# Performance work log

Hardware: AMD Instinct MI355X
Metric: run time of the kernel (lower is better)

The kernel has to match this reference:

```python
import jax, jax.numpy as jnp
import numpy as np

B, N, M, D, H, DH, DFF, L = 64, 2048, 32, 128, 4, 32, 512, 2
EPS = 1e-5


def setup_inputs() -> dict:
    key = jax.random.key(0)
    ks = jax.random.split(key, 8)
    def xav(k, shape, fan_in):
        return jax.random.normal(k, shape, jnp.float32) * (1.0 / np.sqrt(fan_in))
    return {
        "feat": jax.random.normal(ks[0], (B, N, D), jnp.float32),
        "I_pts": xav(ks[1], (L, M, D), D),                # inducing points per ISAB layer
        "Wq": xav(ks[2], (L, 2, D, H * DH), D),
        "Wk": xav(ks[3], (L, 2, D, H * DH), D),
        "Wv": xav(ks[4], (L, 2, D, H * DH), D),
        "Wo": xav(ks[5], (L, 2, H * DH, D), H * DH),
        "W1": xav(ks[6], (L, 2, D, DFF), D),
        "b1": jnp.zeros((L, 2, DFF), jnp.float32),
        "W2": xav(ks[7], (L, 2, DFF, D), DFF),
        "b2": jnp.zeros((L, 2, D), jnp.float32),
        "ln1_g": jnp.ones((L, 2, D), jnp.float32),
        "ln1_b": jnp.zeros((L, 2, D), jnp.float32),
        "ln2_g": jnp.ones((L, 2, D), jnp.float32),
        "ln2_b": jnp.zeros((L, 2, D), jnp.float32),
    }


def _layer_norm(x, g, b):
    mu = jnp.mean(x, axis=-1, keepdims=True)
    var = jnp.mean(jnp.square(x - mu), axis=-1, keepdims=True)
    return (x - mu) * jax.lax.rsqrt(var + EPS) * g + b


def _mha(q_feat, kv_feat, Wq, Wk, Wv, Wo, W1, b1, W2, b2, g1, be1, g2, be2):
    # q_feat: [B, nq, D], kv_feat: [B, nk, D]
    nq, nk = q_feat.shape[1], kv_feat.shape[1]
    Q = (q_feat @ Wq).reshape(B, nq, H, DH)
    K = (kv_feat @ Wk).reshape(B, nk, H, DH)
    V = (kv_feat @ Wv).reshape(B, nk, H, DH)
    # edge score = sum_d(q*k)/sqrt(d_head); edge_softmax normalizes over kv per query
    scores = jnp.einsum('bqhd,bkhd->bhqk', Q, K) / np.sqrt(DH)
    att = jax.nn.softmax(scores, axis=-1)
    out = jnp.einsum('bhqk,bkhd->bqhd', att, V).reshape(B, nq, H * DH)
    sa = out @ Wo
    x = _layer_norm(q_feat + sa, g1, be1)
    ffn = jax.nn.relu(x @ W1 + b1) @ W2 + b2
    return _layer_norm(x + ffn, g2, be2)


def reference(feat, I_pts, Wq, Wk, Wv, Wo, W1, b1, W2, b2, ln1_g, ln1_b, ln2_g, ln2_b):
    x = feat
    for l in range(L):  # ISAB layers
        query = jnp.broadcast_to(I_pts[l], (B, M, D))
        kv = x
        for j in range(2):  # induced -> set, then set -> induced
            rst = _mha(query, kv,
                       Wq[l, j], Wk[l, j], Wv[l, j], Wo[l, j],
                       W1[l, j], b1[l, j], W2[l, j], b2[l, j],
                       ln1_g[l, j], ln1_b[l, j], ln2_g[l, j], ln2_b[l, j])
            query, kv = kv, rst
        x = rst
    return x
```

## Files before the change

### kernel.cpp

```cpp
#include <hip/hip_runtime.h>
#include <hip/hip_bf16.h>

#define BB 64
#define NN 2048
#define MM 32
#define DD 128
#define HH 4
#define LL 2
#define BN (BB*NN)
#define BM (BB*MM)

typedef short bf16x8 __attribute__((ext_vector_type(8)));
typedef float f32x4 __attribute__((ext_vector_type(4)));
typedef unsigned int u32;
#define MFMA __builtin_amdgcn_mfma_f32_16x16x32_bf16

__device__ __forceinline__ unsigned short f2bf(float f){
  __hip_bfloat16 h = __float2bfloat16(f);
  unsigned short u;
  __builtin_memcpy(&u, &h, 2);
  return u;
}
__device__ __forceinline__ float bf2f(unsigned short u){
  union { u32 u; float f; } v; v.u = ((u32)u) << 16; return v.f;
}
__device__ __forceinline__ u32 pack2(float a, float b){
  return (u32)f2bf(a) | ((u32)f2bf(b) << 16);
}
__device__ __forceinline__ float ldf(const float* p){ return *p; }
__device__ __forceinline__ float ldf(const unsigned short* p){ return bf2f(*p); }
__device__ __forceinline__ void stf(float* p, float v){ *p = v; }
__device__ __forceinline__ void stf(unsigned short* p, float v){ *p = f2bf(v); }

__device__ __forceinline__ f32x4 ld4(const float* p){ return *reinterpret_cast<const f32x4*>(p); }
__device__ __forceinline__ f32x4 ld4(const unsigned short* p){
  ushort4 u = *reinterpret_cast<const ushort4*>(p);
  f32x4 r; r[0]=bf2f(u.x); r[1]=bf2f(u.y); r[2]=bf2f(u.z); r[3]=bf2f(u.w); return r;
}
__device__ __forceinline__ void st4(float* p, f32x4 v){ *reinterpret_cast<f32x4*>(p) = v; }
__device__ __forceinline__ void st4(unsigned short* p, f32x4 v){
  ushort4 u; u.x=f2bf(v[0]); u.y=f2bf(v[1]); u.z=f2bf(v[2]); u.w=f2bf(v[3]);
  *reinterpret_cast<ushort4*>(p) = u;
}

__device__ __forceinline__ bf16x8 cvt8(const float* __restrict__ p){
  float4 a = *reinterpret_cast<const float4*>(p);
  float4 b = *reinterpret_cast<const float4*>(p + 4);
  bf16x8 r;
  r[0]=(short)f2bf(a.x); r[1]=(short)f2bf(a.y); r[2]=(short)f2bf(a.z); r[3]=(short)f2bf(a.w);
  r[4]=(short)f2bf(b.x); r[5]=(short)f2bf(b.y); r[6]=(short)f2bf(b.z); r[7]=(short)f2bf(b.w);
  return r;
}

template<int NW>
__device__ __forceinline__ void stage_img(const unsigned short* __restrict__ img,
                                          unsigned short* Wt){
  int wave = threadIdx.x >> 6, lane = threadIdx.x & 63;
  #pragma unroll
  for (int i = 0; i < 32/NW; i++){
    int off = ((i*NW + wave) << 9);
    const unsigned short* gp = img + off + lane*8;
    unsigned short* lp = Wt + off;
    __builtin_amdgcn_global_load_lds(
        (__attribute__((address_space(1))) void*)gp,
        (__attribute__((address_space(3))) void*)lp, 16, 0, 0);
  }
}

__device__ __forceinline__ bf16x8 bfrag(const unsigned short* Wt, int cb, int k0, int lane){
  int c = (cb << 4) + (lane & 15);
  int kk = (k0 + ((lane >> 4) << 3)) ^ ((c & 7) << 3);
  return *reinterpret_cast<const bf16x8*>(Wt + (c << 7) + kk);
}

__device__ __forceinline__ void load_afrag(const float* __restrict__ A, int r0, int lane,
                                           bf16x8 af[2][4]){
  int li = lane & 15, lg = lane >> 4;
  #pragma unroll
  for (int s = 0; s < 2; s++){
    const float* ap = A + (size_t)(r0 + s*16 + li) * 128 + (lg << 3);
    #pragma unroll
    for (int ks = 0; ks < 4; ks++) af[s][ks] = cvt8(ap + ks*32);
  }
}
__device__ __forceinline__ void load_afrag(const unsigned short* __restrict__ A, int r0,
                                           int lane, bf16x8 af[2][4]){
  int li = lane & 15, lg = lane >> 4;
  #pragma unroll
  for (int s = 0; s < 2; s++){
    const unsigned short* ap = A + (size_t)(r0 + s*16 + li) * 128 + (lg << 3);
    #pragma unroll
    for (int ks = 0; ks < 4; ks++) af[s][ks] = *reinterpret_cast<const bf16x8*>(ap + ks*32);
  }
}

__device__ __forceinline__ void mfma_tile32(const bf16x8 af[2][4], const unsigned short* Wt,
                                            int lane, f32x4 acc[2][8]){
  #pragma unroll
  for (int ks = 0; ks < 4; ks++){
    #pragma unroll
    for (int cb = 0; cb < 8; cb++){
      bf16x8 b = bfrag(Wt, cb, ks*32, lane);
      acc[0][cb] = MFMA(af[0][ks], b, acc[0][cb], 0, 0, 0);
      acc[1][cb] = MFMA(af[1][ks], b, acc[1][cb], 0, 0, 0);
    }
  }
}
__device__ __forceinline__ void mfma_swp(const bf16x8 af[2][4], const unsigned short* Wt,
                                         int lane, f32x4 acc[2][8]){
  #pragma unroll
  for (int ks = 0; ks < 4; ks++){
    #pragma unroll
    for (int cb = 0; cb < 8; cb++){
      bf16x8 w = bfrag(Wt, cb, ks*32, lane);
      acc[0][cb] = MFMA(w, af[0][ks], acc[0][cb], 0, 0, 0);
      acc[1][cb] = MFMA(w, af[1][ks], acc[1][cb], 0, 0, 0);
    }
  }
}

__device__ __forceinline__ void zero_acc(f32x4 acc[2][8]){
  #pragma unroll
  for (int s = 0; s < 2; s++)
    #pragma unroll
    for (int cb = 0; cb < 8; cb++) acc[s][cb] = (f32x4){0.f,0.f,0.f,0.f};
}

__device__ __forceinline__ void store_f32(const f32x4 acc[2][8], float* __restrict__ C,
                                          int r0, int lane){
  int li = lane & 15, lg = lane >> 4;
  #pragma unroll
  for (int s = 0; s < 2; s++)
    #pragma unroll
    for (int q = 0; q < 4; q++){
      float* crow = C + (size_t)(r0 + s*16 + lg*4 + q) * 128;
      #pragma unroll
      for (int cb = 0; cb < 8; cb++) crow[cb*16 + li] = acc[s][cb][q];
    }
}
__device__ __forceinline__ void store_bf16(const f32x4 acc[2][8], unsigned short* __restrict__ C,
                                           int r0, int lane){
  int li = lane & 15, lg = lane >> 4;
  #pragma unroll
  for (int s = 0; s < 2; s++)
    #pragma unroll
    for (int q = 0; q < 4; q++){
      unsigned short* crow = C + (size_t)(r0 + s*16 + lg*4 + q) * 128;
      #pragma unroll
      for (int cb = 0; cb < 8; cb++) crow[cb*16 + li] = f2bf(acc[s][cb][q]);
    }
}
__device__ __forceinline__ void store_st2(const f32x4 acc[2][8], unsigned short* __restrict__ St2,
                                          int b, int jb, int lane){
  int li = lane & 15, lg = lane >> 4;
  #pragma unroll
  for (int s = 0; s < 2; s++)
    #pragma unroll
    for (int cb = 0; cb < 8; cb++){
      unsigned short* p = St2 + ((size_t)(b*128 + cb*16 + li))*2048 + jb + s*16 + lg*4;
      st4(p, acc[s][cb]);
    }
}

template<typename RT, typename OT>
__device__ __forceinline__ void ln_ep(const f32x4 acc[8], const float* __restrict__ bias,
    const RT* __restrict__ resid, unsigned int resmask,
    const float* __restrict__ g, const float* __restrict__ beta,
    OT* __restrict__ C, int r0, int lane){
  int li = lane & 15, lg = lane >> 4;
  float gv[8], bv[8], biasv[8];
  #pragma unroll
  for (int cb = 0; cb < 8; cb++){
    int col = cb*16 + li;
    gv[cb] = g[col]; bv[cb] = beta[col];
    biasv[cb] = bias ? bias[col] : 0.f;
  }
  #pragma unroll
  for (int q = 0; q < 4; q++){
    int r = r0 + lg*4 + q;
    const RT* rrow = resid + (size_t)(r & resmask) * 128;
    float v[8], sum = 0.f, ss = 0.f;
    #pragma unroll
    for (int cb = 0; cb < 8; cb++){
      float x = acc[cb][q] + biasv[cb] + ldf(rrow + cb*16 + li);
      v[cb] = x; sum += x; ss += x*x;
    }
    #pragma unroll
    for (int mk = 1; mk < 16; mk <<= 1){ sum += __shfl_xor(sum, mk); ss += __shfl_xor(ss, mk); }
    float mu = sum * (1.f/128.f);
    float var = ss * (1.f/128.f) - mu*mu;
    float rs = rsqrtf(var + 1e-5f);
    OT* crow = C + (size_t)r * 128;
    #pragma unroll
    for (int cb = 0; cb < 8; cb++)
      stf(crow + cb*16 + li, (v[cb] - mu) * rs * gv[cb] + bv[cb]);
  }
}

template<typename RT, typename OT>
__device__ __forceinline__ void ln_swp(const f32x4 accO[2][8], const float* __restrict__ bias,
    const RT* __restrict__ resid, const float* __restrict__ g, const float* __restrict__ beta,
    OT* __restrict__ C, int r0, int lane){
  int li = lane & 15, lg = lane >> 4;
  #pragma unroll
  for (int s = 0; s < 2; s++){
    int r = r0 + s*16 + li;
    const RT* rr = resid + (size_t)r * 128;
    float v[8][4]; float sum = 0.f, ss = 0.f;
    #pragma unroll
    for (int cb = 0; cb < 8; cb++){
      int c0 = cb*16 + lg*4;
      f32x4 rq = ld4(rr + c0);
      f32x4 bq = bias ? *reinterpret_cast<const f32x4*>(bias + c0) : (f32x4){0.f,0.f,0.f,0.f};
      #pragma unroll
      for (int q = 0; q < 4; q++){
        float x = accO[s][cb][q] + bq[q] + rq[q];
        v[cb][q] = x; sum += x; ss += x*x;
      }
    }
    sum += __shfl_xor(sum, 16); ss += __shfl_xor(ss, 16);
    sum += __shfl_xor(sum, 32); ss += __shfl_xor(ss, 32);
    float mu = sum * (1.f/128.f);
    float var = ss * (1.f/128.f) - mu*mu;
    float rs = rsqrtf(var + 1e-5f);
    OT* co = C + (size_t)r * 128;
    #pragma unroll
    for (int cb = 0; cb < 8; cb++){
      int c0 = cb*16 + lg*4;
      f32x4 gq = *reinterpret_cast<const f32x4*>(g + c0);
      f32x4 tq = *reinterpret_cast<const f32x4*>(beta + c0);
      f32x4 o;
      #pragma unroll
      for (int q = 0; q < 4; q++) o[q] = (v[cb][q] - mu) * rs * gq[q] + tq[q];
      st4(co + c0, o);
    }
  }
}

__device__ __forceinline__ bf16x8 redist(const u32 pk[2][8][2], int s, int ks,
                                         int t, int srcA, int srcB){
  u32 a0 = (u32)__shfl((int)pk[s][2*ks][0],   srcA);
  u32 a1 = (u32)__shfl((int)pk[s][2*ks+1][0], srcA);
  u32 a2 = (u32)__shfl((int)pk[s][2*ks][1],   srcA);
  u32 a3 = (u32)__shfl((int)pk[s][2*ks+1][1], srcA);
  u32 b0 = (u32)__shfl((int)pk[s][2*ks][0],   srcB);
  u32 b1 = (u32)__shfl((int)pk[s][2*ks+1][0], srcB);
  u32 b2 = (u32)__shfl((int)pk[s][2*ks][1],   srcB);
  u32 b3 = (u32)__shfl((int)pk[s][2*ks+1][1], srcB);
  union { u32 u[4]; bf16x8 v; } r;
  r.u[0] = t ? a1 : a0;
  r.u[1] = t ? a3 : a2;
  r.u[2] = t ? b1 : b0;
  r.u[3] = t ? b3 : b2;
  return r.v;
}


__global__ __launch_bounds__(256) void cvt_bf16(const float* __restrict__ in,
                                                unsigned short* __restrict__ out){
  size_t i = ((size_t)blockIdx.x*256 + threadIdx.x) * 8;
  float4 a = *reinterpret_cast<const float4*>(in + i);
  float4 b = *reinterpret_cast<const float4*>(in + i + 4);
  ushort4 u0; u0.x=f2bf(a.x); u0.y=f2bf(a.y); u0.z=f2bf(a.z); u0.w=f2bf(a.w);
  ushort4 u1; u1.x=f2bf(b.x); u1.y=f2bf(b.y); u1.z=f2bf(b.z); u1.w=f2bf(b.w);
  *reinterpret_cast<ushort4*>(out + i) = u0;
  *reinterpret_cast<ushort4*>(out + i + 4) = u1;
}

__global__ __launch_bounds__(256) void prep_imgs(const float* __restrict__ Wq,
    const float* __restrict__ Wk, const float* __restrict__ Wv, const float* __restrict__ Wo,
    const float* __restrict__ W1, const float* __restrict__ W2, unsigned short* __restrict__ imgs){
  int slot = blockIdx.x;
  const float* src; int ldw;
  if (slot < 16){
    int j = slot >> 2, m = slot & 3;
    const float* base = (m==0) ? Wq : (m==1) ? Wk : (m==2) ? Wv : Wo;
    src = base + j*16384; ldw = 128;
  } else if (slot < 32){
    int s = slot - 16; int j = s >> 2, dc = s & 3;
    src = W1 + j*65536 + dc*128; ldw = 512;
  } else {
    int s = slot - 32; int j = s >> 2, dc = s & 3;
    src = W2 + j*65536 + dc*16384; ldw = 128;
  }
  unsigned short* img = imgs + (size_t)slot * 16384;
  for (int i = threadIdx.x; i < 16384; i += 256){
    int k = i >> 7, c = i & 127;
    img[(c << 7) + (k ^ ((c & 7) << 3))] = f2bf(src[k*ldw + c]);
  }
}

__global__ __launch_bounds__(256) void prep_phaseA(const float* __restrict__ I,
    const float* __restrict__ Wq, const float* __restrict__ Wk, unsigned short* __restrict__ WfImg){
  __shared__ float Qi[32*128];
  for (int i = threadIdx.x; i < 4096; i += 256){
    int q = i >> 7, c = i & 127;
    float s = 0.f;
    #pragma unroll 8
    for (int d = 0; d < 128; d++) s += I[q*128 + d] * Wq[d*128 + c];
    Qi[i] = s;
  }
  __syncthreads();
  const float scale = 0.17677669529663687f;
  for (int i = threadIdx.x; i < 1024; i += 256){
    int k = (blockIdx.x << 3) + (i >> 7), c = i & 127;
    int hc = c >> 5, qc = c & 31;
    float s = 0.f;
    #pragma unroll
    for (int d = 0; d < 32; d++) s += Wk[k*128 + hc*32 + d] * Qi[qc*128 + hc*32 + d];
    WfImg[(c << 7) + (k ^ ((c & 7) << 3))] = f2bf(s * scale);
  }
}

__global__ __launch_bounds__(256) void prep_phaseB(const float* __restrict__ Wq,
    const float* __restrict__ Wo, const float* __restrict__ Khb, const float* __restrict__ Vhb,
    unsigned short* __restrict__ WfImgs, unsigned short* __restrict__ GvImgs){
  __shared__ float Ks[32*129];
  __shared__ float Vs[32*129];
  __shared__ float Wqt[128*33];
  __shared__ float Wot[128*17];
  int b = blockIdx.x >> 3, part = blockIdx.x & 7;
  int hwf = part >> 1;
  for (int i = threadIdx.x; i < 4096; i += 256){
    int k = i >> 7, c = i & 127;
    Ks[k*129 + c] = Khb[b*4096 + i];
    Vs[k*129 + c] = Vhb[b*4096 + i];
  }
  for (int i = threadIdx.x; i < 4096; i += 256){
    int ci = i >> 5, d = i & 31;
    Wqt[ci*33 + d] = Wq[ci*128 + hwf*32 + d];
  }
  for (int i = threadIdx.x; i < 2048; i += 256){
    int row = i >> 4, cl = i & 15;
    Wot[row*17 + cl] = Wo[row*128 + part*16 + cl];
  }
  __syncthreads();
  const float scale = 0.17677669529663687f;
  unsigned short* wf = WfImgs + (size_t)b*16384;
  unsigned short* gv = GvImgs + (size_t)b*16384;
  {
    int ci = threadIdx.x & 127;
    float wq[32];
    #pragma unroll
    for (int d = 0; d < 32; d++) wq[d] = Wqt[ci*33 + d];
    #pragma unroll
    for (int it = 0; it < 8; it++){
      int kp = part*16 + (threadIdx.x >> 7) + it*2;
      int k = kp & 31;
      float s = 0.f;
      #pragma unroll
      for (int d = 0; d < 32; d++) s += wq[d] * Ks[k*129 + hwf*32 + d];
      wf[(kp << 7) + (ci ^ ((kp & 7) << 3))] = f2bf(s * scale);
    }
  }
  {
    int kp = threadIdx.x & 127;
    int h = kp >> 5, k = kp & 31;
    float vv[32];
    #pragma unroll
    for (int d = 0; d < 32; d++) vv[d] = Vs[k*129 + h*32 + d];
    #pragma unroll
    for (int it = 0; it < 8; it++){
      int c = part*16 + (threadIdx.x >> 7) + it*2;
      int cl = c & 15;
      float s = 0.f;
      #pragma unroll
      for (int d = 0; d < 32; d++) s += vv[d] * Wot[(h*32 + d)*17 + cl];
      gv[(c << 7) + (kp ^ ((c & 7) << 3))] = f2bf(s);
    }
  }
}

template<typename TX>
__global__ __launch_bounds__(512) void gemm_dual(const TX* __restrict__ X,
    const unsigned short* __restrict__ img0, const unsigned short* __restrict__ img1,
    unsigned short* __restrict__ St2, unsigned short* __restrict__ Vb){
  __shared__ __align__(16) unsigned short W0[16384];
  __shared__ __align__(16) unsigned short W1s[16384];
  stage_img<8>(img0, W0);
  stage_img<8>(img1, W1s);
  __syncthreads();
  int lane = threadIdx.x & 63, wave = threadIdx.x >> 6;
  int r0 = blockIdx.x*256 + wave*32;
  int b = r0 >> 11, jb = r0 & 2047;
  bf16x8 af[2][4];
  load_afrag(X, r0, lane, af);
  f32x4 acc[2][8];
  zero_acc(acc);
  mfma_tile32(af, W0, lane, acc);
  store_st2(acc, St2, b, jb, lane);
  zero_acc(acc);
  mfma_tile32(af, W1s, lane, acc);
  store_bf16(acc, Vb, r0, lane);
}

__global__ __launch_bounds__(256) void gemm_img(const float* __restrict__ A,
    const unsigned short* __restrict__ img, float* __restrict__ C){
  __shared__ __align__(16) unsigned short Wt[16384];
  stage_img<4>(img, Wt);
  __syncthreads();
  int lane = threadIdx.x & 63, wave = threadIdx.x >> 6;
  int r0 = blockIdx.x*128 + wave*32;
  bf16x8 af[2][4];
  load_afrag(A, r0, lane, af);
  f32x4 acc[2][8];
  zero_acc(acc);
  mfma_tile32(af, Wt, lane, acc);
  store_f32(acc, C, r0, lane);
}

__global__ __launch_bounds__(256) void gemm_ln_f32A(const float* __restrict__ A,
    const unsigned short* __restrict__ img, const float* __restrict__ resid, unsigned int resmask,
    const float* __restrict__ g, const float* __restrict__ beta, float* __restrict__ C){
  __shared__ __align__(16) unsigned short Wt[16384];
  stage_img<4>(img, Wt);
  __syncthreads();
  int lane = threadIdx.x & 63, wave = threadIdx.x >> 6;
  int r0 = blockIdx.x*128 + wave*32;
  bf16x8 af[2][4];
  load_afrag(A, r0, lane, af);
  f32x4 acc[2][8];
  zero_acc(acc);
  mfma_tile32(af, Wt, lane, acc);
  ln_ep(acc[0], nullptr, resid, resmask, g, beta, C, r0,      lane);
  ln_ep(acc[1], nullptr, resid, resmask, g, beta, C, r0 + 16, lane);
}

__global__ __launch_bounds__(512) void attn_pv(const unsigned short* __restrict__ St2,
    const unsigned short* __restrict__ V, float* __restrict__ O){
  __shared__ __align__(16) unsigned short Vt[2][4096];
  __shared__ __align__(16) float Ocomb[4][64][4];
  __shared__ float scomb[4][16];
  int b = blockIdx.x >> 2, h = blockIdx.x & 3;
  int lane = threadIdx.x & 63, w = threadIdx.x >> 6;
  int li = lane & 15, lg = lane >> 4;
  int qh = w & 1, dh = (w >> 1) & 1, jh = w >> 2;
  int tq = w & 3;
  const unsigned short* Sp = St2 + ((size_t)(b*128 + h*32 + qh*16 + li)) * 2048 + jh*1024;
  const unsigned short* Vb = V + (size_t)b*NN*128 + h*32;
  unsigned short* VtJ = Vt[jh];
  int vrow = tq*32 + (lane >> 2);
  int vd0  = (lane & 3) * 8;
  const unsigned short* vsrc = Vb + ((size_t)(jh*1024 + vrow))*128 + vd0;

  f32x4 acc = (f32x4){0.f,0.f,0.f,0.f};
  float s = 0.f;
  bf16x8 Ar[2][4];
  bf16x8 vr[2][2];

  #pragma unroll
  for (int t = 0; t < 2; t++)
    vr[0][t] = *reinterpret_cast<const bf16x8*>(vsrc + (size_t)t*16*128);
  #pragma unroll
  for (int ks = 0; ks < 4; ks++)
    Ar[0][ks] = *reinterpret_cast<const bf16x8*>(Sp + ks*32 + lg*8);

  #pragma unroll
  for (int c = 0; c < 8; c++){
    const int cur = c & 1, nxt = cur ^ 1;
    __syncthreads();
    #pragma unroll
    for (int t = 0; t < 2; t++){
      int jl = vrow + t*16;
      #pragma unroll
      for (int e = 0; e < 8; e++){
        int d = vd0 + e;
        VtJ[(d << 7) + (jl ^ ((d & 7) << 3))] = (unsigned short)vr[cur][t][e];
      }
    }
    __syncthreads();
    if (c < 7){
      #pragma unroll
      for (int t = 0; t < 2; t++)
        vr[nxt][t] = *reinterpret_cast<const bf16x8*>(vsrc + ((size_t)(c+1)*128 + t*16)*128);
      #pragma unroll
      for (int ks = 0; ks < 4; ks++)
        Ar[nxt][ks] = *reinterpret_cast<const bf16x8*>(Sp + (c+1)*128 + ks*32 + lg*8);
    }
    #pragma unroll
    for (int ks = 0; ks < 4; ks++){
      bf16x8 a;
      #pragma unroll
      for (int e = 0; e < 8; e++){
        float pv = __expf(fminf(bf2f((unsigned short)Ar[cur][ks][e]), 60.f));
        s += pv; a[e] = (short)f2bf(pv);
      }
      bf16x8 bb = bfrag(VtJ, dh, ks*32, lane);
      acc = MFMA(a, bb, acc, 0, 0, 0);
    }
  }
  s += __shfl_xor(s, 16);
  s += __shfl_xor(s, 32);
  if (jh == 1){
    *reinterpret_cast<f32x4*>(&Ocomb[tq][lane][0]) = acc;
    if (lg == 0) scomb[tq][li] = s;
  }
  __syncthreads();
  if (jh == 0){
    acc += *reinterpret_cast<const f32x4*>(&Ocomb[tq][lane][0]);
    float inv = 1.f / (s + scomb[tq][li]);
    float* op = O + ((size_t)(b*MM + qh*16))*128 + h*32 + dh*16 + li;
    #pragma unroll
    for (int r = 0; r < 4; r++){
      float iv = __shfl(inv, lg*4 + r);
      op[(size_t)(lg*4 + r)*128] = acc[r] * iv;
    }
  }
}

template<typename TX>
__global__ __launch_bounds__(512, 2) void attn_swp(const TX* __restrict__ X,
    const unsigned short* __restrict__ WfImgs, const unsigned short* __restrict__ GvImgs,
    const float* __restrict__ g, const float* __restrict__ beta,
    unsigned short* __restrict__ X1){
  __shared__ __align__(16) unsigned short WtF[16384];
  __shared__ __align__(16) unsigned short WtG[16384];
  int b = blockIdx.x >> 3;
  stage_img<8>(WfImgs + (size_t)b*16384, WtF);
  stage_img<8>(GvImgs + (size_t)b*16384, WtG);
  int lane = threadIdx.x & 63, wave = threadIdx.x >> 6;
  int li = lane & 15, lg = lane >> 4;
  int r0 = blockIdx.x*256 + wave*32;
  bf16x8 af[2][4];
  load_afrag(X, r0, lane, af);
  __syncthreads();
  f32x4 sv[2][8];
  zero_acc(sv);
  mfma_swp(af, WtF, lane, sv);
  u32 pk[2][8][2];
  #pragma unroll
  for (int s = 0; s < 2; s++)
    #pragma unroll
    for (int h = 0; h < 4; h++){
      float p[8];
      #pragma unroll
      for (int q = 0; q < 4; q++){ p[q] = sv[s][2*h][q]; p[4+q] = sv[s][2*h+1][q]; }
      float m = fmaxf(fmaxf(fmaxf(p[0],p[1]),fmaxf(p[2],p[3])),
                      fmaxf(fmaxf(p[4],p[5]),fmaxf(p[6],p[7])));
      m = fmaxf(m, __shfl_xor(m, 16));
      m = fmaxf(m, __shfl_xor(m, 32));
      float sm = 0.f;
      #pragma unroll
      for (int i = 0; i < 8; i++){ p[i] = __expf(p[i] - m); sm += p[i]; }
      sm += __shfl_xor(sm, 16);
      sm += __shfl_xor(sm, 32);
      float inv = 1.f / sm;
      pk[s][2*h][0]   = pack2(p[0]*inv, p[1]*inv);
      pk[s][2*h][1]   = pack2(p[2]*inv, p[3]*inv);
      pk[s][2*h+1][0] = pack2(p[4]*inv, p[5]*inv);
      pk[s][2*h+1][1] = pack2(p[6]*inv, p[7]*inv);
    }
  int t = lg >> 1;
  int srcA = li + (((lane >> 4) & 1) << 5);
  int srcB = srcA + 16;
  f32x4 accO[2][8];
  zero_acc(accO);
  #pragma unroll
  for (int ks = 0; ks < 4; ks++){
    bf16x8 hb0 = redist(pk, 0, ks, t, srcA, srcB);
    bf16x8 hb1 = redist(pk, 1, ks, t, srcA, srcB);
    #pragma unroll
    for (int cb = 0; cb < 8; cb++){
      bf16x8 w = bfrag(WtG, cb, ks*32, lane);
      accO[0][cb] = MFMA(w, hb0, accO[0][cb], 0, 0, 0);
      accO[1][cb] = MFMA(w, hb1, accO[1][cb], 0, 0, 0);
    }
  }
  ln_swp(accO, nullptr, X, g, beta, X1, r0, lane);
}

template<typename TA, typename TO>
__global__ __launch_bounds__(512, 2) void ffn_swp(const TA* __restrict__ X,
    const unsigned short* __restrict__ W1i, const float* __restrict__ b1,
    const unsigned short* __restrict__ W2i, const float* __restrict__ b2,
    const float* __restrict__ g, const float* __restrict__ beta,
    TO* __restrict__ OUT){
  __shared__ __align__(16) unsigned short Wt0[16384];
  __shared__ __align__(16) unsigned short Wt1[16384];
  int lane = threadIdx.x & 63, wave = threadIdx.x >> 6;
  int li = lane & 15, lg = lane >> 4;
  int r0 = blockIdx.x*256 + wave*32;
  bf16x8 af[2][4];
  load_afrag(X, r0, lane, af);
  f32x4 accO[2][8];
  zero_acc(accO);
  stage_img<8>(W1i, Wt0);
  stage_img<8>(W2i, Wt1);
  __syncthreads();
  int t = lg >> 1;
  int srcA = li + (((lane >> 4) & 1) << 5);
  int srcB = srcA + 16;
  for (int dc = 0; dc < 4; dc++){
    f32x4 acc1[2][8];
    zero_acc(acc1);
    mfma_swp(af, Wt0, lane, acc1);
    u32 pk[2][8][2];
    #pragma unroll
    for (int s = 0; s < 2; s++)
      #pragma unroll
      for (int cb = 0; cb < 8; cb++){
        f32x4 bq = *reinterpret_cast<const f32x4*>(b1 + dc*128 + cb*16 + lg*4);
        float v0 = fmaxf(acc1[s][cb][0] + bq[0], 0.f);
        float v1 = fmaxf(acc1[s][cb][1] + bq[1], 0.f);
        float v2 = fmaxf(acc1[s][cb][2] + bq[2], 0.f);
        float v3 = fmaxf(acc1[s][cb][3] + bq[3], 0.f);
        pk[s][cb][0] = pack2(v0, v1);
        pk[s][cb][1] = pack2(v2, v3);
      }
    __syncthreads();
    if (dc < 3) stage_img<8>(W1i + (dc+1)*16384, Wt0);
    #pragma unroll
    for (int ks = 0; ks < 4; ks++){
      bf16x8 hb0 = redist(pk, 0, ks, t, srcA, srcB);
      bf16x8 hb1 = redist(pk, 1, ks, t, srcA, srcB);
      #pragma unroll
      for (int cb = 0; cb < 8; cb++){
        bf16x8 w = bfrag(Wt1, cb, ks*32, lane);
        accO[0][cb] = MFMA(w, hb0, accO[0][cb], 0, 0, 0);
        accO[1][cb] = MFMA(w, hb1, accO[1][cb], 0, 0, 0);
      }
    }
    __syncthreads();
    if (dc < 3) stage_img<8>(W2i + (dc+1)*16384, Wt1);
  }
  ln_swp(accO, b2, X, g, beta, OUT, r0, lane);
}

extern "C" void kernel_launch(void* const* d_in, const int* in_sizes, int n_in,
                              void* d_out, int out_size, void* d_ws, size_t ws_size,
                              hipStream_t stream){
  (void)in_sizes; (void)n_in; (void)out_size;
  const float* feat = (const float*)d_in[0];
  const float* Ipts = (const float*)d_in[1];
  const float* Wq   = (const float*)d_in[2];
  const float* Wk   = (const float*)d_in[3];
  const float* Wv   = (const float*)d_in[4];
  const float* Wo   = (const float*)d_in[5];
  const float* W1   = (const float*)d_in[6];
  const float* b1   = (const float*)d_in[7];
  const float* W2   = (const float*)d_in[8];
  const float* b2   = (const float*)d_in[9];
  const float* g1   = (const float*)d_in[10];
  const float* be1  = (const float*)d_in[11];
  const float* g2   = (const float*)d_in[12];
  const float* be2  = (const float*)d_in[13];
  float* out = (float*)d_out;

  unsigned short* St2  = (unsigned short*)d_ws;
  unsigned short* bigX1 = St2;
  unsigned short* bigV = St2 + (size_t)BN*128;
  float* Oind  = (float*)(bigV + (size_t)BN*128);
  float* x1ind = Oind  + (size_t)BM*128;
  float* Hind  = x1ind + (size_t)BM*128;
  float* Khb   = Hind  + (size_t)BM*128;
  float* Vhb   = Khb   + (size_t)BM*128;
  unsigned short* imgs = (unsigned short*)(Vhb + (size_t)BM*128);

  unsigned short* imgQKVO = imgs;
  unsigned short* imgW1   = imgs + (size_t)16*16384;
  unsigned short* imgW2   = imgs + (size_t)32*16384;
  unsigned short* imgWf   = imgs + (size_t)48*16384;
  unsigned short* wfB     = imgs + (size_t)50*16384;
  unsigned short* gvB     = imgs + (size_t)114*16384;
  unsigned short* xb      = imgs + (size_t)178*16384;
  size_t need = (size_t)((char*)(xb + (size_t)BN*128) - (char*)d_ws);
  bool useXb = (ws_size >= need);

  prep_imgs<<<48, 256, 0, stream>>>(Wq, Wk, Wv, Wo, W1, W2, imgs);
  if (useXb)
    cvt_bf16<<<BN*128/8/256, 256, 0, stream>>>(feat, xb);

  for (int l = 0; l < LL; l++){
    const float* xf = (l == 0) ? feat : out;
    bool xBf = useXb;
    const float* Il = Ipts + l*MM*DD;
    int j0 = l*2, j1 = l*2 + 1;
    prep_phaseA<<<16, 256, 0, stream>>>(Il, Wq + j0*16384, Wk + j0*16384, imgWf + l*16384);
    if (xBf)
      gemm_dual<unsigned short><<<BN/256, 512, 0, stream>>>(xb, imgWf + l*16384,
          imgQKVO + (j0*4+2)*16384, St2, bigV);
    else
      gemm_dual<float><<<BN/256, 512, 0, stream>>>(xf, imgWf + l*16384,
          imgQKVO + (j0*4+2)*16384, St2, bigV);
    attn_pv<<<BB*HH, 512, 0, stream>>>(St2, bigV, Oind);
    gemm_ln_f32A<<<BM/128, 256, 0, stream>>>(Oind, imgQKVO + (j0*4+3)*16384, Il, 31u,
                                             g1 + j0*128, be1 + j0*128, x1ind);
    ffn_swp<float, float><<<BM/256, 512, 0, stream>>>(x1ind, imgW1 + (size_t)j0*4*16384,
        b1 + j0*512, imgW2 + (size_t)j0*4*16384, b2 + j0*128,
        g2 + j0*128, be2 + j0*128, Hind);
    gemm_img<<<BM/128, 256, 0, stream>>>(Hind, imgQKVO + (j1*4+1)*16384, Khb);
    gemm_img<<<BM/128, 256, 0, stream>>>(Hind, imgQKVO + (j1*4+2)*16384, Vhb);
    prep_phaseB<<<BB*8, 256, 0, stream>>>(Wq + j1*16384, Wo + j1*16384, Khb, Vhb, wfB, gvB);
    if (xBf)
      attn_swp<unsigned short><<<BN/256, 512, 0, stream>>>(xb, wfB, gvB,
          g1 + j1*128, be1 + j1*128, bigX1);
    else
      attn_swp<float><<<BN/256, 512, 0, stream>>>(xf, wfB, gvB,
          g1 + j1*128, be1 + j1*128, bigX1);
    if (l == 0 && useXb)
      ffn_swp<unsigned short, unsigned short><<<BN/256, 512, 0, stream>>>(bigX1,
          imgW1 + (size_t)j1*4*16384, b1 + j1*512, imgW2 + (size_t)j1*4*16384, b2 + j1*128,
          g2 + j1*128, be2 + j1*128, xb);
    else
      ffn_swp<unsigned short, float><<<BN/256, 512, 0, stream>>>(bigX1,
          imgW1 + (size_t)j1*4*16384, b1 + j1*512, imgW2 + (size_t)j1*4*16384, b2 + j1*128,
          g2 + j1*128, be2 + j1*128, out);
  }
}
```

Before: 552.8 us.

## Fuse set-side attention and FFN into one kernel, keeping x1 in registers

Merges the attn_swp and ffn_swp kernels for the N-sized set into a single attn_ffn kernel. The post-attention LayerNorm output is packed to bf16 in registers and fed straight into the FFN as both the GEMM A-operand and the residual. This removes the global write and re-read of the intermediate bigX1 buffer, and one kernel launch. In exchange, it holds extra packed state (pkX1) live across the FFN loop, which raises register pressure under the 512-thread, 2-block launch bounds and could cause spills.

```diff
diff --git a/kernel.cpp b/kernel.cpp
--- a/kernel.cpp
+++ b/kernel.cpp
@@ -508,67 +508,6 @@
   }
 }
 
-template<typename TX>
-__global__ __launch_bounds__(512, 2) void attn_swp(const TX* __restrict__ X,
-    const unsigned short* __restrict__ WfImgs, const unsigned short* __restrict__ GvImgs,
-    const float* __restrict__ g, const float* __restrict__ beta,
-    unsigned short* __restrict__ X1){
-  __shared__ __align__(16) unsigned short WtF[16384];
-  __shared__ __align__(16) unsigned short WtG[16384];
-  int b = blockIdx.x >> 3;
-  stage_img<8>(WfImgs + (size_t)b*16384, WtF);
-  stage_img<8>(GvImgs + (size_t)b*16384, WtG);
-  int lane = threadIdx.x & 63, wave = threadIdx.x >> 6;
-  int li = lane & 15, lg = lane >> 4;
-  int r0 = blockIdx.x*256 + wave*32;
-  bf16x8 af[2][4];
-  load_afrag(X, r0, lane, af);
-  __syncthreads();
-  f32x4 sv[2][8];
-  zero_acc(sv);
-  mfma_swp(af, WtF, lane, sv);
-  u32 pk[2][8][2];
-  #pragma unroll
-  for (int s = 0; s < 2; s++)
-    #pragma unroll
-    for (int h = 0; h < 4; h++){
-      float p[8];
-      #pragma unroll
-      for (int q = 0; q < 4; q++){ p[q] = sv[s][2*h][q]; p[4+q] = sv[s][2*h+1][q]; }
-      float m = fmaxf(fmaxf(fmaxf(p[0],p[1]),fmaxf(p[2],p[3])),
-                      fmaxf(fmaxf(p[4],p[5]),fmaxf(p[6],p[7])));
-      m = fmaxf(m, __shfl_xor(m, 16));
-      m = fmaxf(m, __shfl_xor(m, 32));
-      float sm = 0.f;
-      #pragma unroll
-      for (int i = 0; i < 8; i++){ p[i] = __expf(p[i] - m); sm += p[i]; }
-      sm += __shfl_xor(sm, 16);
-      sm += __shfl_xor(sm, 32);
-      float inv = 1.f / sm;
-      pk[s][2*h][0]   = pack2(p[0]*inv, p[1]*inv);
-      pk[s][2*h][1]   = pack2(p[2]*inv, p[3]*inv);
-      pk[s][2*h+1][0] = pack2(p[4]*inv, p[5]*inv);
-      pk[s][2*h+1][1] = pack2(p[6]*inv, p[7]*inv);
-    }
-  int t = lg >> 1;
-  int srcA = li + (((lane >> 4) & 1) << 5);
-  int srcB = srcA + 16;
-  f32x4 accO[2][8];
-  zero_acc(accO);
-  #pragma unroll
-  for (int ks = 0; ks < 4; ks++){
-    bf16x8 hb0 = redist(pk, 0, ks, t, srcA, srcB);
-    bf16x8 hb1 = redist(pk, 1, ks, t, srcA, srcB);
-    #pragma unroll
-    for (int cb = 0; cb < 8; cb++){
-      bf16x8 w = bfrag(WtG, cb, ks*32, lane);
-      accO[0][cb] = MFMA(w, hb0, accO[0][cb], 0, 0, 0);
-      accO[1][cb] = MFMA(w, hb1, accO[1][cb], 0, 0, 0);
-    }
-  }
-  ln_swp(accO, nullptr, X, g, beta, X1, r0, lane);
-}
-
 template<typename TA, typename TO>
 __global__ __launch_bounds__(512, 2) void ffn_swp(const TA* __restrict__ X,
     const unsigned short* __restrict__ W1i, const float* __restrict__ b1,
@@ -624,6 +563,178 @@
     if (dc < 3) stage_img<8>(W2i + (dc+1)*16384, Wt1);
   }
   ln_swp(accO, b2, X, g, beta, OUT, r0, lane);
+}
+
+template<typename TX, typename TO>
+__global__ __launch_bounds__(512, 2) void attn_ffn(const TX* __restrict__ X,
+    const unsigned short* __restrict__ WfImgs, const unsigned short* __restrict__ GvImgs,
+    const float* __restrict__ g1v, const float* __restrict__ be1v,
+    const unsigned short* __restrict__ W1i, const float* __restrict__ b1,
+    const unsigned short* __restrict__ W2i, const float* __restrict__ b2,
+    const float* __restrict__ g2v, const float* __restrict__ be2v,
+    TO* __restrict__ OUT){
+  __shared__ __align__(16) unsigned short Wt0[16384];
+  __shared__ __align__(16) unsigned short Wt1[16384];
+  int b = blockIdx.x >> 3;
+  stage_img<8>(WfImgs + (size_t)b*16384, Wt0);
+  stage_img<8>(GvImgs + (size_t)b*16384, Wt1);
+  int lane = threadIdx.x & 63, wave = threadIdx.x >> 6;
+  int li = lane & 15, lg = lane >> 4;
+  int r0 = blockIdx.x*256 + wave*32;
+  int t = lg >> 1;
+  int srcA = li + (((lane >> 4) & 1) << 5);
+  int srcB = srcA + 16;
+  bf16x8 af[2][4];
+  load_afrag(X, r0, lane, af);
+  __syncthreads();
+  f32x4 accO[2][8];
+  zero_acc(accO);
+  mfma_swp(af, Wt0, lane, accO);
+  u32 pkP[2][8][2];
+  #pragma unroll
+  for (int s = 0; s < 2; s++)
+    #pragma unroll
+    for (int h = 0; h < 4; h++){
+      float p[8];
+      #pragma unroll
+      for (int q = 0; q < 4; q++){ p[q] = accO[s][2*h][q]; p[4+q] = accO[s][2*h+1][q]; }
+      float m = fmaxf(fmaxf(fmaxf(p[0],p[1]),fmaxf(p[2],p[3])),
+                      fmaxf(fmaxf(p[4],p[5]),fmaxf(p[6],p[7])));
+      m = fmaxf(m, __shfl_xor(m, 16));
+      m = fmaxf(m, __shfl_xor(m, 32));
+      float sm = 0.f;
+      #pragma unroll
+      for (int i = 0; i < 8; i++){ p[i] = __expf(p[i] - m); sm += p[i]; }
+      sm += __shfl_xor(sm, 16);
+      sm += __shfl_xor(sm, 32);
+      float inv = 1.f / sm;
+      pkP[s][2*h][0]   = pack2(p[0]*inv, p[1]*inv);
+      pkP[s][2*h][1]   = pack2(p[2]*inv, p[3]*inv);
+      pkP[s][2*h+1][0] = pack2(p[4]*inv, p[5]*inv);
+      pkP[s][2*h+1][1] = pack2(p[6]*inv, p[7]*inv);
+    }
+  zero_acc(accO);
+  #pragma unroll
+  for (int ks = 0; ks < 4; ks++){
+    bf16x8 hb0 = redist(pkP, 0, ks, t, srcA, srcB);
+    bf16x8 hb1 = redist(pkP, 1, ks, t, srcA, srcB);
+    #pragma unroll
+    for (int cb = 0; cb < 8; cb++){
+      bf16x8 w = bfrag(Wt1, cb, ks*32, lane);
+      accO[0][cb] = MFMA(w, hb0, accO[0][cb], 0, 0, 0);
+      accO[1][cb] = MFMA(w, hb1, accO[1][cb], 0, 0, 0);
+    }
+  }
+  __syncthreads();
+  stage_img<8>(W1i, Wt0);
+  stage_img<8>(W2i, Wt1);
+  u32 pkX1[2][8][2];
+  #pragma unroll
+  for (int s = 0; s < 2; s++){
+    int r = r0 + s*16 + li;
+    const TX* rr = X + (size_t)r * 128;
+    float v[8][4]; float sum = 0.f, ss = 0.f;
+    #pragma unroll
+    for (int cb = 0; cb < 8; cb++){
+      int c0 = cb*16 + lg*4;
+      f32x4 rq = ld4(rr + c0);
+      #pragma unroll
+      for (int q = 0; q < 4; q++){
+        float x = accO[s][cb][q] + rq[q];
+        v[cb][q] = x; sum += x; ss += x*x;
+      }
+    }
+    sum += __shfl_xor(sum, 16); ss += __shfl_xor(ss, 16);
+    sum += __shfl_xor(sum, 32); ss += __shfl_xor(ss, 32);
+    float mu = sum * (1.f/128.f);
+    float var = ss * (1.f/128.f) - mu*mu;
+    float rs = rsqrtf(var + 1e-5f);
+    #pragma unroll
+    for (int cb = 0; cb < 8; cb++){
+      int c0 = cb*16 + lg*4;
+      f32x4 gq = *reinterpret_cast<const f32x4*>(g1v + c0);
+      f32x4 tq = *reinterpret_cast<const f32x4*>(be1v + c0);
+      float x0 = (v[cb][0] - mu)*rs*gq[0] + tq[0];
+      float x1 = (v[cb][1] - mu)*rs*gq[1] + tq[1];
+      float x2 = (v[cb][2] - mu)*rs*gq[2] + tq[2];
+      float x3 = (v[cb][3] - mu)*rs*gq[3] + tq[3];
+      pkX1[s][cb][0] = pack2(x0, x1);
+      pkX1[s][cb][1] = pack2(x2, x3);
+    }
+  }
+  bf16x8 af2[2][4];
+  #pragma unroll
+  for (int s = 0; s < 2; s++)
+    #pragma unroll
+    for (int ks = 0; ks < 4; ks++)
+      af2[s][ks] = redist(pkX1, s, ks, t, srcA, srcB);
+  __syncthreads();
+  zero_acc(accO);
+  for (int dc = 0; dc < 4; dc++){
+    f32x4 acc1[2][8];
+    zero_acc(acc1);
+    mfma_swp(af2, Wt0, lane, acc1);
+    u32 pk[2][8][2];
+    #pragma unroll
+    for (int s = 0; s < 2; s++)
+      #pragma unroll
+      for (int cb = 0; cb < 8; cb++){
+        f32x4 bq = *reinterpret_cast<const f32x4*>(b1 + dc*128 + cb*16 + lg*4);
+        float v0 = fmaxf(acc1[s][cb][0] + bq[0], 0.f);
+        float v1 = fmaxf(acc1[s][cb][1] + bq[1], 0.f);
+        float v2 = fmaxf(acc1[s][cb][2] + bq[2], 0.f);
+        float v3 = fmaxf(acc1[s][cb][3] + bq[3], 0.f);
+        pk[s][cb][0] = pack2(v0, v1);
+        pk[s][cb][1] = pack2(v2, v3);
+      }
+    __syncthreads();
+    if (dc < 3) stage_img<8>(W1i + (dc+1)*16384, Wt0);
+    #pragma unroll
+    for (int ks = 0; ks < 4; ks++){
+      bf16x8 hb0 = redist(pk, 0, ks, t, srcA, srcB);
+      bf16x8 hb1 = redist(pk, 1, ks, t, srcA, srcB);
+      #pragma unroll
+      for (int cb = 0; cb < 8; cb++){
+        bf16x8 w = bfrag(Wt1, cb, ks*32, lane);
+        accO[0][cb] = MFMA(w, hb0, accO[0][cb], 0, 0, 0);
+        accO[1][cb] = MFMA(w, hb1, accO[1][cb], 0, 0, 0);
+      }
+    }
+    __syncthreads();
+    if (dc < 3) stage_img<8>(W2i + (dc+1)*16384, Wt1);
+  }
+  #pragma unroll
+  for (int s = 0; s < 2; s++){
+    int r = r0 + s*16 + li;
+    float v[8][4]; float sum = 0.f, ss = 0.f;
+    #pragma unroll
+    for (int cb = 0; cb < 8; cb++){
+      int c0 = cb*16 + lg*4;
+      f32x4 bq = *reinterpret_cast<const f32x4*>(b2 + c0);
+      #pragma unroll
+      for (int q = 0; q < 4; q++){
+        float resid = bf2f((unsigned short)((pkX1[s][cb][q>>1] >> ((q&1)*16)) & 0xFFFFu));
+        float x = accO[s][cb][q] + bq[q] + resid;
+        v[cb][q] = x; sum += x; ss += x*x;
+      }
+    }
+    sum += __shfl_xor(sum, 16); ss += __shfl_xor(ss, 16);
+    sum += __shfl_xor(sum, 32); ss += __shfl_xor(ss, 32);
+    float mu = sum * (1.f/128.f);
+    float var = ss * (1.f/128.f) - mu*mu;
+    float rs = rsqrtf(var + 1e-5f);
+    TO* co = OUT + (size_t)r * 128;
+    #pragma unroll
+    for (int cb = 0; cb < 8; cb++){
+      int c0 = cb*16 + lg*4;
+      f32x4 gq = *reinterpret_cast<const f32x4*>(g2v + c0);
+      f32x4 tq = *reinterpret_cast<const f32x4*>(be2v + c0);
+      f32x4 o;
+      #pragma unroll
+      for (int q = 0; q < 4; q++) o[q] = (v[cb][q] - mu) * rs * gq[q] + tq[q];
+      st4(co + c0, o);
+    }
+  }
 }
 
 extern "C" void kernel_launch(void* const* d_in, const int* in_sizes, int n_in,
@@ -647,7 +758,6 @@
   float* out = (float*)d_out;
 
   unsigned short* St2  = (unsigned short*)d_ws;
-  unsigned short* bigX1 = St2;
   unsigned short* bigV = St2 + (size_t)BN*128;
   float* Oind  = (float*)(bigV + (size_t)BN*128);
   float* x1ind = Oind  + (size_t)BM*128;
@@ -691,19 +801,17 @@
     gemm_img<<<BM/128, 256, 0, stream>>>(Hind, imgQKVO + (j1*4+1)*16384, Khb);
     gemm_img<<<BM/128, 256, 0, stream>>>(Hind, imgQKVO + (j1*4+2)*16384, Vhb);
     prep_phaseB<<<BB*8, 256, 0, stream>>>(Wq + j1*16384, Wo + j1*16384, Khb, Vhb, wfB, gvB);
-    if (xBf)
-      attn_swp<unsigned short><<<BN/256, 512, 0, stream>>>(xb, wfB, gvB,
-          g1 + j1*128, be1 + j1*128, bigX1);
+    if (l == 0 && useXb)
+      attn_ffn<unsigned short, unsigned short><<<BN/256, 512, 0, stream>>>(xb, wfB, gvB,
+          g1 + j1*128, be1 + j1*128, imgW1 + (size_t)j1*4*16384, b1 + j1*512,
+          imgW2 + (size_t)j1*4*16384, b2 + j1*128, g2 + j1*128, be2 + j1*128, xb);
+    else if (useXb)
+      attn_ffn<unsigned short, float><<<BN/256, 512, 0, stream>>>(xb, wfB, gvB,
+          g1 + j1*128, be1 + j1*128, imgW1 + (size_t)j1*4*16384, b1 + j1*512,
+          imgW2 + (size_t)j1*4*16384, b2 + j1*128, g2 + j1*128, be2 + j1*128, out);
     else
-      attn_swp<float><<<BN/256, 512, 0, stream>>>(xf, wfB, gvB,
-          g1 + j1*128, be1 + j1*128, bigX1);
-    if (l == 0 && useXb)
-      ffn_swp<unsigned short, unsigned short><<<BN/256, 512, 0, stream>>>(bigX1,
-          imgW1 + (size_t)j1*4*16384, b1 + j1*512, imgW2 + (size_t)j1*4*16384, b2 + j1*128,
-          g2 + j1*128, be2 + j1*128, xb);
-    else
-      ffn_swp<unsigned short, float><<<BN/256, 512, 0, stream>>>(bigX1,
-          imgW1 + (size_t)j1*4*16384, b1 + j1*512, imgW2 + (size_t)j1*4*16384, b2 + j1*128,
-          g2 + j1*128, be2 + j1*128, out);
-  }
-}
+      attn_ffn<float, float><<<BN/256, 512, 0, stream>>>(xf, wfB, gvB,
+          g1 + j1*128, be1 + j1*128, imgW1 + (size_t)j1*4*16384, b1 + j1*512,
+          imgW2 + (size_t)j1*4*16384, b2 + j1*128, g2 + j1*128, be2 + j1*128, out);
+  }
+}
```

Measured after the change: 597.7 us. +8.1%, slower.
